# Optimization experiments

Hardware: AMD Instinct MI355X
Metric: run time of the kernel (lower is better)

The kernel has to match this reference:

```python
import jax, jax.numpy as jnp
import numpy as np

N_NODES = 50000
N_EDGES = 800000
D_IN, D_HID, D_OUT = 128, 128, 64
BN_EPS = 1e-5


def gcn_conv(x, W, b, src, dst, ew, n):
    # PyG GCNConv: out[i] = sum_j norm_ij * (x @ W)[j] + b, with self-loops added
    xw = x @ W                                   # [N, D_out]
    loop = jnp.arange(n)
    s = jnp.concatenate([src, loop])             # add self-loops (weight 1)
    d = jnp.concatenate([dst, loop])
    w = jnp.concatenate([ew, jnp.ones((n,), x.dtype)])
    deg = jax.ops.segment_sum(w, d, num_segments=n)
    dinv = jnp.where(deg > 0, jax.lax.rsqrt(deg), 0.0)
    norm = dinv[s] * w * dinv[d]                 # symmetric normalization
    msg = xw[s] * norm[:, None]                  # gather + scale  [E+N, D_out]
    return jax.ops.segment_sum(msg, d, num_segments=n) + b


def setup_inputs() -> dict:
    key = jax.random.key(0)
    ks = jax.random.split(key, 12)
    x = jax.random.normal(ks[0], (N_NODES, D_IN), dtype=jnp.float32)
    edge_index = jax.random.randint(ks[1], (2, N_EDGES), 0, N_NODES, dtype=jnp.int64)
    edge_weight = jax.random.uniform(ks[2], (N_EDGES,), dtype=jnp.float32)
    W1 = jax.random.normal(ks[3], (D_IN, D_HID), dtype=jnp.float32) * 0.05
    b1 = jnp.zeros((D_HID,), jnp.float32)
    gamma = jnp.ones((D_HID,), jnp.float32)
    beta = jnp.zeros((D_HID,), jnp.float32)
    running_mean = jax.random.normal(ks[4], (D_HID,), dtype=jnp.float32) * 0.1
    running_var = jax.random.uniform(ks[5], (D_HID,), dtype=jnp.float32) + 0.5
    W2 = jax.random.normal(ks[6], (D_HID, D_OUT), dtype=jnp.float32) * 0.05
    b2 = jnp.zeros((D_OUT,), jnp.float32)
    return {"x": x, "edge_index": edge_index, "edge_weight": edge_weight,
            "W1": W1, "b1": b1, "gamma": gamma, "beta": beta,
            "running_mean": running_mean, "running_var": running_var,
            "W2": W2, "b2": b2}


def reference(x, edge_index, edge_weight, W1, b1, gamma, beta,
              running_mean, running_var, W2, b2):
    src, dst = edge_index[0], edge_index[1]
    n = x.shape[0]
    h = gcn_conv(x, W1, b1, src, dst, edge_weight, n)
    # BatchNorm1d in eval mode (running stats); dropout inactive in eval
    h = (h - running_mean) * jax.lax.rsqrt(running_var + BN_EPS) * gamma + beta
    h = jax.nn.relu(h)
    out = gcn_conv(h, W2, b2, src, dst, edge_weight, n)
    return out
```

## Files before the change

kernel.cpp:

```cpp
#include <hip/hip_runtime.h>
#include <hip/hip_fp16.h>

#define BN_EPS 1e-5f
#define PAD 64
#define CAP 4608

typedef __attribute__((ext_vector_type(8))) short short8;
typedef __attribute__((ext_vector_type(4))) float f32x4;

static __device__ __forceinline__ unsigned short f2bf(float f) {
    unsigned u = __float_as_uint(f);
    u += 0x7FFF + ((u >> 16) & 1);
    return (unsigned short)(u >> 16);
}
static __device__ __forceinline__ float bf2f(unsigned short b) {
    return __uint_as_float((unsigned)b << 16);
}
static __device__ __forceinline__ unsigned pk(int s, float w) {
    return ((unsigned)s << 16) | (unsigned)__half_as_ushort(__float2half_rn(w));
}
static __device__ __forceinline__ float pw(unsigned e) {
    return __half2float(__ushort_as_half((unsigned short)(e & 0xFFFFu)));
}
static __device__ __forceinline__ void upk8(uint4 v, float4& a, float4& b) {
    a.x = bf2f((unsigned short)(v.x & 0xFFFFu)); a.y = bf2f((unsigned short)(v.x >> 16));
    a.z = bf2f((unsigned short)(v.y & 0xFFFFu)); a.w = bf2f((unsigned short)(v.y >> 16));
    b.x = bf2f((unsigned short)(v.z & 0xFFFFu)); b.y = bf2f((unsigned short)(v.z >> 16));
    b.z = bf2f((unsigned short)(v.w & 0xFFFFu)); b.w = bf2f((unsigned short)(v.w >> 16));
}
#define FMA8(wv, ra, rb, A, B)                                            \
    A.x += (wv) * ra.x; A.y += (wv) * ra.y; A.z += (wv) * ra.z; A.w += (wv) * ra.w; \
    B.x += (wv) * rb.x; B.y += (wv) * rb.y; B.z += (wv) * rb.z; B.w += (wv) * rb.w;

__global__ __launch_bounds__(256) void k_fused(const int* __restrict__ src, const int* __restrict__ dst,
                                               const float* __restrict__ ew,
                                               uint2* __restrict__ bins, int* __restrict__ gcnt,
                                               int e, int gfill, int stride, int nb,
                                               const float* __restrict__ A, const float* __restrict__ W,
                                               unsigned short* __restrict__ C, int n,
                                               const float* __restrict__ b1, const float* __restrict__ gamma,
                                               const float* __restrict__ beta, const float* __restrict__ mean,
                                               const float* __restrict__ var,
                                               float* __restrict__ bnscale, float* __restrict__ bnshift,
                                               const float* __restrict__ W2, unsigned short* __restrict__ w2bf) {
    __shared__ unsigned short W1s[8192];
    int tid = threadIdx.x;
    int b = (int)blockIdx.x;
    int gGemm = ((n + 63) / 64) * 2;

    bool isFill = ((b % stride) == 0) && (b / stride < gfill);
    if (isFill) {
        int*   lcnt   = (int*)W1s;
        int*   gbase  = lcnt + 256;
        int*   loff   = gbase + 256;
        uint2* sorted = (uint2*)(loff + 256);
        lcnt[tid] = 0;
        __syncthreads();

        int i0 = ((b / stride) * 256 + tid) * 4;
        unsigned pv[4];  int bk[4]; int rk[4]; unsigned dl[4];
        int cnt4 = 0;
        if (i0 + 3 < e) {
            int4   s0 = *(const int4*)(src + i0);
            int4   d0 = *(const int4*)(dst + i0);
            float4 w0 = *(const float4*)(ew + i0);
            int   ss[4] = {s0.x, s0.y, s0.z, s0.w};
            int   dd[4] = {d0.x, d0.y, d0.z, d0.w};
            float ww[4] = {w0.x, w0.y, w0.z, w0.w};
            #pragma unroll
            for (int j = 0; j < 4; ++j) {
                int d_ = dd[j];
                bk[j] = d_ >> 8;
                dl[j] = (unsigned)(d_ & 255);
                rk[j] = atomicAdd(&lcnt[bk[j]], 1);
                pv[j] = pk(ss[j], ww[j]);
            }
            cnt4 = 4;
        } else {
            for (int j = 0; j < 4; ++j) {
                int i = i0 + j;
                if (i < e) {
                    int d_ = dst[i];
                    bk[j] = d_ >> 8;
                    dl[j] = (unsigned)(d_ & 255);
                    rk[j] = atomicAdd(&lcnt[bk[j]], 1);
                    pv[j] = pk(src[i], ew[i]);
                    cnt4 = j + 1;
                }
            }
        }
        __syncthreads();
        if (tid < nb) gbase[tid] = atomicAdd(&gcnt[tid], lcnt[tid]);
        int li = lcnt[tid];
        loff[tid] = li;
        __syncthreads();
        #pragma unroll
        for (int off = 1; off < 256; off <<= 1) {
            int v = (tid >= off) ? loff[tid - off] : 0;
            __syncthreads();
            loff[tid] += v;
            __syncthreads();
        }
        int excl = loff[tid] - li;
        __syncthreads();
        loff[tid] = excl;
        __syncthreads();
        for (int j = 0; j < cnt4; ++j) {
            int pos  = gbase[bk[j]] + rk[j];
            int sidx = loff[bk[j]] + rk[j];
            unsigned gp = (pos < CAP) ? ((unsigned)(bk[j] * CAP + pos) | (dl[j] << 24))
                                      : 0xFFFFFFFFu;
            sorted[sidx] = make_uint2(pv[j], gp);
        }
        __syncthreads();
        int total = loff[255] + lcnt[255];
        for (int i = tid; i < total; i += 256) {
            uint2 s = sorted[i];
            if (s.y != 0xFFFFFFFFu)
                bins[s.y & 0x00FFFFFFu] = make_uint2(s.x, s.y >> 24);
        }
        return;
    }

    int fillsBefore = (b == 0) ? 0 : min(gfill, (b - 1) / stride + 1);
    int g = b - fillsBefore;
    if (g == gGemm) {
        if (tid < 128) {
            float sc = gamma[tid] * rsqrtf(var[tid] + BN_EPS);
            bnscale[tid] = sc;
            bnshift[tid] = (b1[tid] - mean[tid]) * sc + beta[tid];
        }
        #pragma unroll
        for (int q = 0; q < 4; ++q) {
            int s = tid * 4 + q;
            int kk = s >> 8, nt = (s >> 6) & 3, lane = s & 63;
            int kb = kk * 32 + ((lane >> 4) << 3);
            int nc = (nt << 4) + (lane & 15);
            ushort4 o0, o1;
            o0.x = f2bf(W2[(kb + 0) * 64 + nc]);
            o0.y = f2bf(W2[(kb + 1) * 64 + nc]);
            o0.z = f2bf(W2[(kb + 2) * 64 + nc]);
            o0.w = f2bf(W2[(kb + 3) * 64 + nc]);
            o1.x = f2bf(W2[(kb + 4) * 64 + nc]);
            o1.y = f2bf(W2[(kb + 5) * 64 + nc]);
            o1.z = f2bf(W2[(kb + 6) * 64 + nc]);
            o1.w = f2bf(W2[(kb + 7) * 64 + nc]);
            ((ushort4*)w2bf)[s * 2]     = o0;
            ((ushort4*)w2bf)[s * 2 + 1] = o1;
        }
        return;
    }

    int rt = g >> 1, ch = g & 1;
    int row0 = rt * 64, c0 = ch * 64;

    {
        int k  = tid >> 1;
        int h0 = (tid & 1) * 32;
        int kk = k >> 5, lg = (k >> 3) & 3, ii = k & 7;
        int tbase = kk * 2048 + lg * 128 + ii;
        const float4* Wr = (const float4*)(W + (size_t)k * 128 + c0 + h0);
        #pragma unroll
        for (int j = 0; j < 8; ++j) {
            float4 v = Wr[j];
            int n0 = h0 + j * 4;
            W1s[tbase + ((n0 + 0) >> 4) * 512 + ((n0 + 0) & 15) * 8] = f2bf(v.x);
            W1s[tbase + ((n0 + 1) >> 4) * 512 + ((n0 + 1) & 15) * 8] = f2bf(v.y);
            W1s[tbase + ((n0 + 2) >> 4) * 512 + ((n0 + 2) & 15) * 8] = f2bf(v.z);
            W1s[tbase + ((n0 + 3) >> 4) * 512 + ((n0 + 3) & 15) * 8] = f2bf(v.w);
        }
    }
    __syncthreads();

    int w = tid >> 6, lane = tid & 63;
    int arow = row0 + w * 16 + (lane & 15);
    if (arow > n - 1) arow = n - 1;
    const float* xrow = A + (size_t)arow * 128 + ((lane >> 4) * 8);
    const unsigned short* Wl = W1s + (size_t)lane * 8;

    f32x4 z = {0.f, 0.f, 0.f, 0.f};
    f32x4 acc0 = z, acc1 = z, acc2 = z, acc3 = z;

    #pragma unroll
    for (int kk = 0; kk < 4; ++kk) {
        float4 v0 = *(const float4*)(xrow + kk * 32);
        float4 v1 = *(const float4*)(xrow + kk * 32 + 4);
        short8 a;
        a[0] = (short)f2bf(v0.x); a[1] = (short)f2bf(v0.y);
        a[2] = (short)f2bf(v0.z); a[3] = (short)f2bf(v0.w);
        a[4] = (short)f2bf(v1.x); a[5] = (short)f2bf(v1.y);
        a[6] = (short)f2bf(v1.z); a[7] = (short)f2bf(v1.w);
        const unsigned short* Wk = Wl + kk * 2048;
        short8 b0 = *(const short8*)(Wk);
        short8 b1 = *(const short8*)(Wk + 512);
        short8 b2 = *(const short8*)(Wk + 1024);
        short8 b3 = *(const short8*)(Wk + 1536);
        acc0 = __builtin_amdgcn_mfma_f32_16x16x32_bf16(a, b0, acc0, 0, 0, 0);
        acc1 = __builtin_amdgcn_mfma_f32_16x16x32_bf16(a, b1, acc1, 0, 0, 0);
        acc2 = __builtin_amdgcn_mfma_f32_16x16x32_bf16(a, b2, acc2, 0, 0, 0);
        acc3 = __builtin_amdgcn_mfma_f32_16x16x32_bf16(a, b3, acc3, 0, 0, 0);
    }

    int rw = row0 + w * 16 + ((lane >> 4) << 2);
    int cb = c0 + (lane & 15);
    #define STORE_NT(av, nt)                                                              \
        if (rw + 0 < n) C[(size_t)(rw + 0) * 128 + (nt)*16 + cb] = f2bf(av[0]);           \
        if (rw + 1 < n) C[(size_t)(rw + 1) * 128 + (nt)*16 + cb] = f2bf(av[1]);           \
        if (rw + 2 < n) C[(size_t)(rw + 2) * 128 + (nt)*16 + cb] = f2bf(av[2]);           \
        if (rw + 3 < n) C[(size_t)(rw + 3) * 128 + (nt)*16 + cb] = f2bf(av[3]);
    STORE_NT(acc0, 0) STORE_NT(acc1, 1) STORE_NT(acc2, 2) STORE_NT(acc3, 3)
    #undef STORE_NT
}

__global__ __launch_bounds__(256) void k_csr(const uint2* __restrict__ bins, const int* __restrict__ gcnt,
                                             unsigned* __restrict__ pad, int* __restrict__ cnt,
                                             float* __restrict__ dinv, int n) {
    __shared__ unsigned csr[256 * PAD];
    __shared__ int lc[256];
    int tid = threadIdx.x;
    int b = (int)blockIdx.x;
    int node0 = b << 8;
    int nodes = min(256, n - node0);
    lc[tid] = 0;
    __syncthreads();

    int m = gcnt[b];
    if (m > CAP) m = CAP;
    const uint2* seg = bins + (size_t)b * CAP;
    for (int i = tid; i < m; i += 256) {
        uint2 v = seg[i];
        int r = atomicAdd(&lc[v.y], 1);
        if (r < PAD) csr[v.y * PAD + r] = v.x;
    }
    __syncthreads();

    if (tid < nodes) {
        int c = lc[tid];
        cnt[node0 + tid] = c;
        int cc = min(c, PAD);
        float s = 1.0f;
        for (int p = 0; p < cc; ++p) s += pw(csr[tid * PAD + p]);
        dinv[node0 + tid] = rsqrtf(s);
    }
    const uint4* s4 = (const uint4*)csr;
    uint4* d4 = (uint4*)(pad + (size_t)node0 * PAD);
    int tot = nodes * (PAD / 4);
    for (int q = tid; q < tot; q += 256) d4[q] = s4[q];
}

__global__ __launch_bounds__(256) void k_scale(unsigned* __restrict__ pad, const int* __restrict__ cnt,
                                               const float* __restrict__ dinv, int n) {
    int gid = blockIdx.x * 256 + threadIdx.x;
    int node = gid >> 2, q = gid & 3;
    if (node >= n) return;
    int c = min(cnt[node], PAD);
    int p0 = q * 16, p1 = min(p0 + 16, c);
    size_t base = (size_t)node * PAD;
    for (int p = p0; p < p1; ++p) {
        unsigned e = pad[base + p];
        float w = pw(e) * dinv[e >> 16];
        pad[base + p] = (e & 0xFFFF0000u) | (unsigned)__half_as_ushort(__float2half_rn(w));
    }
}

__global__ __launch_bounds__(256) void k_h(const unsigned short* __restrict__ xw, const int* __restrict__ cnt,
                                           const unsigned* __restrict__ pad,
                                           const float* __restrict__ dinv,
                                           const float* __restrict__ scale, const float* __restrict__ shift,
                                           unsigned* __restrict__ h, int n) {
    int grp = threadIdx.x >> 4;
    int lc  = threadIdx.x & 15;
    int node = blockIdx.x * 16 + grp;
    if (node >= n) return;
    const uint4* X = (const uint4*)xw;
    float di = dinv[node];
    int c = min(cnt[node], PAD);
    size_t base = (size_t)node * PAD;
    float4 ra, rb;
    upk8(X[(size_t)node * 16 + lc], ra, rb);
    float4 A0 = make_float4(ra.x * di, ra.y * di, ra.z * di, ra.w * di);
    float4 B0 = make_float4(rb.x * di, rb.y * di, rb.z * di, rb.w * di);
    float4 A1 = make_float4(0, 0, 0, 0), B1 = A1;
    float4 A2 = A1, B2 = A1, A3 = A1, B3 = A1;
    int p = 0;
    for (; p + 3 < c; p += 4) {
        uint4 ee = *(const uint4*)(pad + base + p);
        uint4 r0 = X[(size_t)(ee.x >> 16) * 16 + lc];
        uint4 r1 = X[(size_t)(ee.y >> 16) * 16 + lc];
        uint4 r2 = X[(size_t)(ee.z >> 16) * 16 + lc];
        uint4 r3 = X[(size_t)(ee.w >> 16) * 16 + lc];
        float w0 = pw(ee.x), w1 = pw(ee.y), w2 = pw(ee.z), w3 = pw(ee.w);
        float4 a, b;
        upk8(r0, a, b); FMA8(w0, a, b, A0, B0);
        upk8(r1, a, b); FMA8(w1, a, b, A1, B1);
        upk8(r2, a, b); FMA8(w2, a, b, A2, B2);
        upk8(r3, a, b); FMA8(w3, a, b, A3, B3);
    }
    for (; p < c; ++p) {
        unsigned e0 = pad[base + p];
        float w0 = pw(e0);
        float4 a, b;
        upk8(X[(size_t)(e0 >> 16) * 16 + lc], a, b);
        FMA8(w0, a, b, A0, B0);
    }
    A0.x = (A0.x + A1.x + A2.x + A3.x) * di;
    A0.y = (A0.y + A1.y + A2.y + A3.y) * di;
    A0.z = (A0.z + A1.z + A2.z + A3.z) * di;
    A0.w = (A0.w + A1.w + A2.w + A3.w) * di;
    B0.x = (B0.x + B1.x + B2.x + B3.x) * di;
    B0.y = (B0.y + B1.y + B2.y + B3.y) * di;
    B0.z = (B0.z + B1.z + B2.z + B3.z) * di;
    B0.w = (B0.w + B1.w + B2.w + B3.w) * di;
    float4 Sc0 = ((const float4*)scale)[lc * 2];
    float4 Sc1 = ((const float4*)scale)[lc * 2 + 1];
    float4 Sh0 = ((const float4*)shift)[lc * 2];
    float4 Sh1 = ((const float4*)shift)[lc * 2 + 1];
    unsigned short h0 = f2bf(fmaxf(A0.x * Sc0.x + Sh0.x, 0.0f));
    unsigned short h1 = f2bf(fmaxf(A0.y * Sc0.y + Sh0.y, 0.0f));
    unsigned short h2 = f2bf(fmaxf(A0.z * Sc0.z + Sh0.z, 0.0f));
    unsigned short h3 = f2bf(fmaxf(A0.w * Sc0.w + Sh0.w, 0.0f));
    unsigned short h4 = f2bf(fmaxf(B0.x * Sc1.x + Sh1.x, 0.0f));
    unsigned short h5 = f2bf(fmaxf(B0.y * Sc1.y + Sh1.y, 0.0f));
    unsigned short h6 = f2bf(fmaxf(B0.z * Sc1.z + Sh1.z, 0.0f));
    unsigned short h7 = f2bf(fmaxf(B0.w * Sc1.w + Sh1.w, 0.0f));
    uint4 o;
    o.x = ((unsigned)h1 << 16) | h0;
    o.y = ((unsigned)h3 << 16) | h2;
    o.z = ((unsigned)h5 << 16) | h4;
    o.w = ((unsigned)h7 << 16) | h6;
    ((uint4*)h)[(size_t)node * 16 + lc] = o;
}

__global__ __launch_bounds__(256) void k_gemm2(const unsigned short* __restrict__ h,
                                               const unsigned short* __restrict__ w2bf,
                                               unsigned short* __restrict__ hw2, int n) {
    __shared__ unsigned short W2f[8192];
    int tid = threadIdx.x;
    {
        const uint4* s4 = (const uint4*)w2bf;
        uint4* d4 = (uint4*)W2f;
        #pragma unroll
        for (int q = 0; q < 4; ++q) d4[q * 256 + tid] = s4[q * 256 + tid];
    }
    __syncthreads();

    int w = tid >> 6, lane = tid & 63;
    int row0 = (int)blockIdx.x * 64 + w * 16;
    int ar = row0 + (lane & 15);
    if (ar > n - 1) ar = n - 1;
    const unsigned short* hr = h + (size_t)ar * 128 + ((lane >> 4) * 8);
    const unsigned short* Wl = W2f + (size_t)lane * 8;

    f32x4 z = {0.f, 0.f, 0.f, 0.f};
    f32x4 acc0 = z, acc1 = z, acc2 = z, acc3 = z;
    #pragma unroll
    for (int kk = 0; kk < 4; ++kk) {
        short8 a = *(const short8*)(hr + kk * 32);
        const unsigned short* Wk = Wl + kk * 2048;
        short8 b0 = *(const short8*)(Wk);
        short8 b1 = *(const short8*)(Wk + 512);
        short8 b2 = *(const short8*)(Wk + 1024);
        short8 b3 = *(const short8*)(Wk + 1536);
        acc0 = __builtin_amdgcn_mfma_f32_16x16x32_bf16(a, b0, acc0, 0, 0, 0);
        acc1 = __builtin_amdgcn_mfma_f32_16x16x32_bf16(a, b1, acc1, 0, 0, 0);
        acc2 = __builtin_amdgcn_mfma_f32_16x16x32_bf16(a, b2, acc2, 0, 0, 0);
        acc3 = __builtin_amdgcn_mfma_f32_16x16x32_bf16(a, b3, acc3, 0, 0, 0);
    }
    int rw = row0 + ((lane >> 4) << 2);
    int cb = lane & 15;
    #define ST_NT(av, nt)                                                                 \
        if (rw + 0 < n) hw2[(size_t)(rw + 0) * 64 + (nt)*16 + cb] = f2bf(av[0]);          \
        if (rw + 1 < n) hw2[(size_t)(rw + 1) * 64 + (nt)*16 + cb] = f2bf(av[1]);          \
        if (rw + 2 < n) hw2[(size_t)(rw + 2) * 64 + (nt)*16 + cb] = f2bf(av[2]);          \
        if (rw + 3 < n) hw2[(size_t)(rw + 3) * 64 + (nt)*16 + cb] = f2bf(av[3]);
    ST_NT(acc0, 0) ST_NT(acc1, 1) ST_NT(acc2, 2) ST_NT(acc3, 3)
    #undef ST_NT
}

__global__ __launch_bounds__(256) void k_agg2(const unsigned short* __restrict__ hw, const int* __restrict__ cnt,
                                              const unsigned* __restrict__ pad,
                                              const float* __restrict__ dinv,
                                              const float* __restrict__ b2, float* __restrict__ out, int n) {
    int node = blockIdx.x * 32 + (threadIdx.x >> 3);
    if (node >= n) return;
    int lc = threadIdx.x & 7;
    const uint4* X = (const uint4*)hw;
    float di = dinv[node];
    int c = min(cnt[node], PAD);
    size_t base = (size_t)node * PAD;
    float4 ra, rb;
    upk8(X[(size_t)node * 8 + lc], ra, rb);
    float4 A0 = make_float4(ra.x * di, ra.y * di, ra.z * di, ra.w * di);
    float4 B0 = make_float4(rb.x * di, rb.y * di, rb.z * di, rb.w * di);
    float4 A1 = make_float4(0, 0, 0, 0), B1 = A1;
    float4 A2 = A1, B2 = A1, A3 = A1, B3 = A1;
    int p = 0;
    for (; p + 3 < c; p += 4) {
        uint4 ee = *(const uint4*)(pad + base + p);
        uint4 r0 = X[(size_t)(ee.x >> 16) * 8 + lc];
        uint4 r1 = X[(size_t)(ee.y >> 16) * 8 + lc];
        uint4 r2 = X[(size_t)(ee.z >> 16) * 8 + lc];
        uint4 r3 = X[(size_t)(ee.w >> 16) * 8 + lc];
        float w0 = pw(ee.x), w1 = pw(ee.y), w2 = pw(ee.z), w3 = pw(ee.w);
        float4 a, b;
        upk8(r0, a, b); FMA8(w0, a, b, A0, B0);
        upk8(r1, a, b); FMA8(w1, a, b, A1, B1);
        upk8(r2, a, b); FMA8(w2, a, b, A2, B2);
        upk8(r3, a, b); FMA8(w3, a, b, A3, B3);
    }
    for (; p < c; ++p) {
        unsigned e0 = pad[base + p];
        float w0 = pw(e0);
        float4 a, b;
        upk8(X[(size_t)(e0 >> 16) * 8 + lc], a, b);
        FMA8(w0, a, b, A0, B0);
    }
    float4 Ba = ((const float4*)b2)[lc * 2];
    float4 Bb = ((const float4*)b2)[lc * 2 + 1];
    float4 o0, o1;
    o0.x = (A0.x + A1.x + A2.x + A3.x) * di + Ba.x;
    o0.y = (A0.y + A1.y + A2.y + A3.y) * di + Ba.y;
    o0.z = (A0.z + A1.z + A2.z + A3.z) * di + Ba.z;
    o0.w = (A0.w + A1.w + A2.w + A3.w) * di + Ba.w;
    o1.x = (B0.x + B1.x + B2.x + B3.x) * di + Bb.x;
    o1.y = (B0.y + B1.y + B2.y + B3.y) * di + Bb.y;
    o1.z = (B0.z + B1.z + B2.z + B3.z) * di + Bb.z;
    o1.w = (B0.w + B1.w + B2.w + B3.w) * di + Bb.w;
    ((float4*)out)[(size_t)node * 16 + lc * 2]     = o0;
    ((float4*)out)[(size_t)node * 16 + lc * 2 + 1] = o1;
}


extern "C" void kernel_launch(void* const* d_in, const int* in_sizes, int n_in,
                              void* d_out, int out_size, void* d_ws, size_t ws_size,
                              hipStream_t stream) {
    const float* x     = (const float*)d_in[0];
    const int*   ei    = (const int*)d_in[1];
    const float* ew    = (const float*)d_in[2];
    const float* W1    = (const float*)d_in[3];
    const float* b1    = (const float*)d_in[4];
    const float* gamma = (const float*)d_in[5];
    const float* beta  = (const float*)d_in[6];
    const float* rmean = (const float*)d_in[7];
    const float* rvar  = (const float*)d_in[8];
    const float* W2    = (const float*)d_in[9];
    const float* b2    = (const float*)d_in[10];
    float* out = (float*)d_out;

    int N = in_sizes[0] / 128;
    int E = in_sizes[2];
    const int* src = ei;
    const int* dst = ei + E;
    int NB = (N + 255) >> 8;

    char* p = (char*)d_ws;
    auto carve = [&](size_t bytes) { char* q = p; p += (bytes + 255) & ~(size_t)255; return (void*)q; };
    int*      cnt     = (int*)     carve(sizeof(int) * (size_t)N);
    unsigned* pad     = (unsigned*)carve(sizeof(unsigned) * (size_t)N * PAD);
    float*    dinv    = (float*)   carve(sizeof(float) * (size_t)N);
    float*    bnscale = (float*)   carve(sizeof(float) * 128);
    float*    bnshift = (float*)   carve(sizeof(float) * 128);
    unsigned short* w2bf = (unsigned short*)carve(sizeof(unsigned short) * 128 * 64);
    unsigned short* xw1  = (unsigned short*)carve(sizeof(unsigned short) * (size_t)N * 128);
    unsigned*       hbuf = (unsigned*)      carve(sizeof(unsigned) * (size_t)N * 64);
    unsigned short* hw2  = (unsigned short*)carve(sizeof(unsigned short) * (size_t)N * 64);
    int*      gcnt    = (int*)     carve(sizeof(int) * (size_t)NB);
    uint2*    bins    = (uint2*)   carve(sizeof(uint2) * (size_t)NB * CAP);

    int gFill = (E + 1023) / 1024;
    int gGemm = ((N + 63) / 64) * 2;
    int T     = gFill + gGemm + 1;
    int S     = T / gFill;
    if (S < 2) S = 2;

    hipMemsetAsync(gcnt, 0, sizeof(int) * (size_t)NB, stream);
    k_fused <<<T, 256, 0, stream>>>(src, dst, ew, bins, gcnt, E, gFill, S, NB,
                                    x, W1, xw1, N,
                                    b1, gamma, beta, rmean, rvar, bnscale, bnshift,
                                    W2, w2bf);
    k_csr   <<<NB, 256, 0, stream>>>(bins, gcnt, pad, cnt, dinv, N);
    k_scale <<<(N * 4 + 255) / 256, 256, 0, stream>>>(pad, cnt, dinv, N);
    k_h     <<<(N + 15) / 16, 256, 0, stream>>>(xw1, cnt, pad, dinv, bnscale, bnshift, hbuf, N);
    k_gemm2 <<<(N + 63) / 64, 256, 0, stream>>>((const unsigned short*)hbuf, w2bf, hw2, N);
    k_agg2  <<<(N + 31) / 32, 256, 0, stream>>>(hw2, cnt, pad, dinv, b2, out, N);
}
```

Baseline: 189.3 us.

## Split aggregation kernels into feature slices with narrower per-thread loads

Both gather-aggregation kernels now split the feature dimension across multiple blocks (4 slices for layer 1, 2 for layer 2), with each thread handling 4 bf16 features via 8-byte loads instead of 8 features via 16-byte loads. This raises the number of threads and waves in flight, which gives more memory-level parallelism for the random row gathers and lowers register use per thread. The cost is that each edge index list is re-read once per slice, and each gathered row is fetched as several smaller segments spread across different blocks.

```diff
diff --git a/kernel.cpp b/kernel.cpp
--- a/kernel.cpp
+++ b/kernel.cpp
@@ -22,15 +22,15 @@
 static __device__ __forceinline__ float pw(unsigned e) {
     return __half2float(__ushort_as_half((unsigned short)(e & 0xFFFFu)));
 }
-static __device__ __forceinline__ void upk8(uint4 v, float4& a, float4& b) {
+static __device__ __forceinline__ float4 upk4(uint2 v) {
+    float4 a;
     a.x = bf2f((unsigned short)(v.x & 0xFFFFu)); a.y = bf2f((unsigned short)(v.x >> 16));
     a.z = bf2f((unsigned short)(v.y & 0xFFFFu)); a.w = bf2f((unsigned short)(v.y >> 16));
-    b.x = bf2f((unsigned short)(v.z & 0xFFFFu)); b.y = bf2f((unsigned short)(v.z >> 16));
-    b.z = bf2f((unsigned short)(v.w & 0xFFFFu)); b.w = bf2f((unsigned short)(v.w >> 16));
-}
-#define FMA8(wv, ra, rb, A, B)                                            \
-    A.x += (wv) * ra.x; A.y += (wv) * ra.y; A.z += (wv) * ra.z; A.w += (wv) * ra.w; \
-    B.x += (wv) * rb.x; B.y += (wv) * rb.y; B.z += (wv) * rb.z; B.w += (wv) * rb.w;
+    return a;
+}
+#define FMA4(wv, rv, A)                                                               \
+    { float4 _t = upk4(rv);                                                           \
+      A.x += (wv) * _t.x; A.y += (wv) * _t.y; A.z += (wv) * _t.z; A.w += (wv) * _t.w; }
 
 __global__ __launch_bounds__(256) void k_fused(const int* __restrict__ src, const int* __restrict__ dst,
                                                const float* __restrict__ ew,
@@ -268,67 +268,53 @@
                                            const float* __restrict__ dinv,
                                            const float* __restrict__ scale, const float* __restrict__ shift,
                                            unsigned* __restrict__ h, int n) {
-    int grp = threadIdx.x >> 4;
-    int lc  = threadIdx.x & 15;
-    int node = blockIdx.x * 16 + grp;
+    int slice = (int)blockIdx.x & 3;
+    int chunk = (int)blockIdx.x >> 2;
+    int grp = threadIdx.x >> 3;
+    int l8  = threadIdx.x & 7;
+    int node = chunk * 32 + grp;
     if (node >= n) return;
-    const uint4* X = (const uint4*)xw;
+    int cu = slice * 8 + l8;
+    const uint2* X = (const uint2*)xw;
     float di = dinv[node];
     int c = min(cnt[node], PAD);
     size_t base = (size_t)node * PAD;
-    float4 ra, rb;
-    upk8(X[(size_t)node * 16 + lc], ra, rb);
-    float4 A0 = make_float4(ra.x * di, ra.y * di, ra.z * di, ra.w * di);
-    float4 B0 = make_float4(rb.x * di, rb.y * di, rb.z * di, rb.w * di);
-    float4 A1 = make_float4(0, 0, 0, 0), B1 = A1;
-    float4 A2 = A1, B2 = A1, A3 = A1, B3 = A1;
+    float4 q = upk4(X[(size_t)node * 32 + cu]);
+    float4 A0 = make_float4(q.x * di, q.y * di, q.z * di, q.w * di);
+    float4 A1 = make_float4(0, 0, 0, 0), A2 = A1, A3 = A1;
     int p = 0;
     for (; p + 3 < c; p += 4) {
         uint4 ee = *(const uint4*)(pad + base + p);
-        uint4 r0 = X[(size_t)(ee.x >> 16) * 16 + lc];
-        uint4 r1 = X[(size_t)(ee.y >> 16) * 16 + lc];
-        uint4 r2 = X[(size_t)(ee.z >> 16) * 16 + lc];
-        uint4 r3 = X[(size_t)(ee.w >> 16) * 16 + lc];
+        uint2 r0 = X[(size_t)(ee.x >> 16) * 32 + cu];
+        uint2 r1 = X[(size_t)(ee.y >> 16) * 32 + cu];
+        uint2 r2 = X[(size_t)(ee.z >> 16) * 32 + cu];
+        uint2 r3 = X[(size_t)(ee.w >> 16) * 32 + cu];
         float w0 = pw(ee.x), w1 = pw(ee.y), w2 = pw(ee.z), w3 = pw(ee.w);
-        float4 a, b;
-        upk8(r0, a, b); FMA8(w0, a, b, A0, B0);
-        upk8(r1, a, b); FMA8(w1, a, b, A1, B1);
-        upk8(r2, a, b); FMA8(w2, a, b, A2, B2);
-        upk8(r3, a, b); FMA8(w3, a, b, A3, B3);
+        FMA4(w0, r0, A0);
+        FMA4(w1, r1, A1);
+        FMA4(w2, r2, A2);
+        FMA4(w3, r3, A3);
     }
     for (; p < c; ++p) {
         unsigned e0 = pad[base + p];
         float w0 = pw(e0);
-        float4 a, b;
-        upk8(X[(size_t)(e0 >> 16) * 16 + lc], a, b);
-        FMA8(w0, a, b, A0, B0);
+        uint2 r0 = X[(size_t)(e0 >> 16) * 32 + cu];
+        FMA4(w0, r0, A0);
     }
     A0.x = (A0.x + A1.x + A2.x + A3.x) * di;
     A0.y = (A0.y + A1.y + A2.y + A3.y) * di;
     A0.z = (A0.z + A1.z + A2.z + A3.z) * di;
     A0.w = (A0.w + A1.w + A2.w + A3.w) * di;
-    B0.x = (B0.x + B1.x + B2.x + B3.x) * di;
-    B0.y = (B0.y + B1.y + B2.y + B3.y) * di;
-    B0.z = (B0.z + B1.z + B2.z + B3.z) * di;
-    B0.w = (B0.w + B1.w + B2.w + B3.w) * di;
-    float4 Sc0 = ((const float4*)scale)[lc * 2];
-    float4 Sc1 = ((const float4*)scale)[lc * 2 + 1];
-    float4 Sh0 = ((const float4*)shift)[lc * 2];
-    float4 Sh1 = ((const float4*)shift)[lc * 2 + 1];
-    unsigned short h0 = f2bf(fmaxf(A0.x * Sc0.x + Sh0.x, 0.0f));
-    unsigned short h1 = f2bf(fmaxf(A0.y * Sc0.y + Sh0.y, 0.0f));
-    unsigned short h2 = f2bf(fmaxf(A0.z * Sc0.z + Sh0.z, 0.0f));
-    unsigned short h3 = f2bf(fmaxf(A0.w * Sc0.w + Sh0.w, 0.0f));
-    unsigned short h4 = f2bf(fmaxf(B0.x * Sc1.x + Sh1.x, 0.0f));
-    unsigned short h5 = f2bf(fmaxf(B0.y * Sc1.y + Sh1.y, 0.0f));
-    unsigned short h6 = f2bf(fmaxf(B0.z * Sc1.z + Sh1.z, 0.0f));
-    unsigned short h7 = f2bf(fmaxf(B0.w * Sc1.w + Sh1.w, 0.0f));
-    uint4 o;
+    float4 Sc = ((const float4*)scale)[cu];
+    float4 Sh = ((const float4*)shift)[cu];
+    unsigned short h0 = f2bf(fmaxf(A0.x * Sc.x + Sh.x, 0.0f));
+    unsigned short h1 = f2bf(fmaxf(A0.y * Sc.y + Sh.y, 0.0f));
+    unsigned short h2 = f2bf(fmaxf(A0.z * Sc.z + Sh.z, 0.0f));
+    unsigned short h3 = f2bf(fmaxf(A0.w * Sc.w + Sh.w, 0.0f));
+    uint2 o;
     o.x = ((unsigned)h1 << 16) | h0;
     o.y = ((unsigned)h3 << 16) | h2;
-    o.z = ((unsigned)h5 << 16) | h4;
-    o.w = ((unsigned)h7 << 16) | h6;
-    ((uint4*)h)[(size_t)node * 16 + lc] = o;
+    ((uint2*)h)[(size_t)node * 32 + cu] = o;
 }
 
 __global__ __launch_bounds__(256) void k_gemm2(const unsigned short* __restrict__ h,
@@ -381,53 +367,46 @@
                                               const unsigned* __restrict__ pad,
                                               const float* __restrict__ dinv,
                                               const float* __restrict__ b2, float* __restrict__ out, int n) {
-    int node = blockIdx.x * 32 + (threadIdx.x >> 3);
+    int slice = (int)blockIdx.x & 1;
+    int chunk = (int)blockIdx.x >> 1;
+    int grp = threadIdx.x >> 3;
+    int l8  = threadIdx.x & 7;
+    int node = chunk * 32 + grp;
     if (node >= n) return;
-    int lc = threadIdx.x & 7;
-    const uint4* X = (const uint4*)hw;
+    int cu = slice * 8 + l8;
+    const uint2* X = (const uint2*)hw;
     float di = dinv[node];
     int c = min(cnt[node], PAD);
     size_t base = (size_t)node * PAD;
-    float4 ra, rb;
-    upk8(X[(size_t)node * 8 + lc], ra, rb);
-    float4 A0 = make_float4(ra.x * di, ra.y * di, ra.z * di, ra.w * di);
-    float4 B0 = make_float4(rb.x * di, rb.y * di, rb.z * di, rb.w * di);
-    float4 A1 = make_float4(0, 0, 0, 0), B1 = A1;
-    float4 A2 = A1, B2 = A1, A3 = A1, B3 = A1;
+    float4 q = upk4(X[(size_t)node * 16 + cu]);
+    float4 A0 = make_float4(q.x * di, q.y * di, q.z * di, q.w * di);
+    float4 A1 = make_float4(0, 0, 0, 0), A2 = A1, A3 = A1;
     int p = 0;
     for (; p + 3 < c; p += 4) {
         uint4 ee = *(const uint4*)(pad + base + p);
-        uint4 r0 = X[(size_t)(ee.x >> 16) * 8 + lc];
-        uint4 r1 = X[(size_t)(ee.y >> 16) * 8 + lc];
-        uint4 r2 = X[(size_t)(ee.z >> 16) * 8 + lc];
-        uint4 r3 = X[(size_t)(ee.w >> 16) * 8 + lc];
+        uint2 r0 = X[(size_t)(ee.x >> 16) * 16 + cu];
+        uint2 r1 = X[(size_t)(ee.y >> 16) * 16 + cu];
+        uint2 r2 = X[(size_t)(ee.z >> 16) * 16 + cu];
+        uint2 r3 = X[(size_t)(ee.w >> 16) * 16 + cu];
         float w0 = pw(ee.x), w1 = pw(ee.y), w2 = pw(ee.z), w3 = pw(ee.w);
-        float4 a, b;
-        upk8(r0, a, b); FMA8(w0, a, b, A0, B0);
-        upk8(r1, a, b); FMA8(w1, a, b, A1, B1);
-        upk8(r2, a, b); FMA8(w2, a, b, A2, B2);
-        upk8(r3, a, b); FMA8(w3, a, b, A3, B3);
+        FMA4(w0, r0, A0);
+        FMA4(w1, r1, A1);
+        FMA4(w2, r2, A2);
+        FMA4(w3, r3, A3);
     }
     for (; p < c; ++p) {
         unsigned e0 = pad[base + p];
         float w0 = pw(e0);
-        float4 a, b;
-        upk8(X[(size_t)(e0 >> 16) * 8 + lc], a, b);
-        FMA8(w0, a, b, A0, B0);
-    }
-    float4 Ba = ((const float4*)b2)[lc * 2];
-    float4 Bb = ((const float4*)b2)[lc * 2 + 1];
-    float4 o0, o1;
-    o0.x = (A0.x + A1.x + A2.x + A3.x) * di + Ba.x;
-    o0.y = (A0.y + A1.y + A2.y + A3.y) * di + Ba.y;
-    o0.z = (A0.z + A1.z + A2.z + A3.z) * di + Ba.z;
-    o0.w = (A0.w + A1.w + A2.w + A3.w) * di + Ba.w;
-    o1.x = (B0.x + B1.x + B2.x + B3.x) * di + Bb.x;
-    o1.y = (B0.y + B1.y + B2.y + B3.y) * di + Bb.y;
-    o1.z = (B0.z + B1.z + B2.z + B3.z) * di + Bb.z;
-    o1.w = (B0.w + B1.w + B2.w + B3.w) * di + Bb.w;
-    ((float4*)out)[(size_t)node * 16 + lc * 2]     = o0;
-    ((float4*)out)[(size_t)node * 16 + lc * 2 + 1] = o1;
+        uint2 r0 = X[(size_t)(e0 >> 16) * 16 + cu];
+        FMA4(w0, r0, A0);
+    }
+    float4 B = ((const float4*)b2)[cu];
+    float4 o;
+    o.x = (A0.x + A1.x + A2.x + A3.x) * di + B.x;
+    o.y = (A0.y + A1.y + A2.y + A3.y) * di + B.y;
+    o.z = (A0.z + A1.z + A2.z + A3.z) * di + B.z;
+    o.w = (A0.w + A1.w + A2.w + A3.w) * di + B.w;
+    ((float4*)out)[(size_t)node * 16 + cu] = o;
 }
 
 
@@ -480,7 +459,7 @@
                                     W2, w2bf);
     k_csr   <<<NB, 256, 0, stream>>>(bins, gcnt, pad, cnt, dinv, N);
     k_scale <<<(N * 4 + 255) / 256, 256, 0, stream>>>(pad, cnt, dinv, N);
-    k_h     <<<(N + 15) / 16, 256, 0, stream>>>(xw1, cnt, pad, dinv, bnscale, bnshift, hbuf, N);
+    k_h     <<<((N + 31) / 32) * 4, 256, 0, stream>>>(xw1, cnt, pad, dinv, bnscale, bnshift, hbuf, N);
     k_gemm2 <<<(N + 63) / 64, 256, 0, stream>>>((const unsigned short*)hbuf, w2bf, hw2, N);
-    k_agg2  <<<(N + 31) / 32, 256, 0, stream>>>(hw2, cnt, pad, dinv, b2, out, N);
-}
+    k_agg2  <<<((N + 31) / 32) * 2, 256, 0, stream>>>(hw2, cnt, pad, dinv, b2, out, N);
+}
```

Result: slower. 212.9 us (+12.5%).
